# Performance work log

Hardware: AMD Instinct MI355X
Metric: run time of the kernel (lower is better)

The kernel has to match this reference:

```python
import jax, jax.numpy as jnp
import numpy as np

CUTOFF = 5.0
N_GAUSS = 25
LOG2 = 0.6931471805599453
N_INTER = 3


def ssp(x):
    # shifted softplus used by SchNet
    return jax.nn.softplus(x) - LOG2


def setup_inputs() -> dict:
    key = jax.random.key(0)
    ks = jax.random.split(key, 16)
    B, A, N, F, G, Z = 16, 128, 127, 128, N_GAUSS, 100
    s = 1.0 / np.sqrt(F)
    emb = jax.random.normal(ks[0], (Z, F), jnp.float32)
    emb = emb.at[0].set(0.0)  # padding_idx=0
    inp = {
        "positions": jax.random.normal(ks[1], (B, A, 3), jnp.float32) * 3.0,
        "cell": jnp.zeros((B, 3, 3), jnp.float32),
        "cell_offset": jnp.zeros((B, A, N, 3), jnp.float32),
        "neighbor_mask": jnp.ones((B, A, N), jnp.float32),
        "embeddings": emb,
        "filt_W1": jax.random.normal(ks[2], (N_INTER, G, F), jnp.float32) / np.sqrt(G),
        "filt_b1": jnp.zeros((N_INTER, F), jnp.float32),
        "filt_W2": jax.random.normal(ks[3], (N_INTER, F, F), jnp.float32) * s,
        "filt_b2": jnp.zeros((N_INTER, F), jnp.float32),
        "in2f_W": jax.random.normal(ks[4], (N_INTER, F, F), jnp.float32) * s,
        "f2out_W": jax.random.normal(ks[5], (N_INTER, F, F), jnp.float32) * s,
        "f2out_b": jnp.zeros((N_INTER, F), jnp.float32),
        "dense_W": jax.random.normal(ks[6], (N_INTER, F, F), jnp.float32) * s,
        "dense_b": jnp.zeros((N_INTER, F), jnp.float32),
        "atomic_numbers": jax.random.randint(ks[7], (B, A), 1, Z).astype(jnp.int32),
        "neighbors": jax.random.randint(ks[8], (B, A, N), 0, A).astype(jnp.int32),
    }
    return inp


def _schnet_forward(positions, cell, cell_offset, neighbor_mask, embeddings,
                    filt_W1, filt_b1, filt_W2, filt_b2,
                    in2f_W, f2out_W, f2out_b, dense_W, dense_b,
                    atomic_numbers, neighbors):
    B, A, _ = positions.shape
    bidx = jnp.arange(B)[:, None, None]

    # ---- AtomDistances: gather neighbor positions, pairwise distances ----
    pos_nbh = positions[bidx, neighbors]            # [B,A,N,3]
    dvec = pos_nbh - positions[:, :, None, :]
    dvec = dvec + jnp.einsum('banj,bjc->banc', cell_offset, cell)
    d2 = jnp.sum(dvec * dvec, axis=-1)              # [B,A,N]
    m = neighbor_mask > 0
    r_ij = jnp.where(m, jnp.sqrt(jnp.where(m, d2, 1.0)), 0.0)

    # ---- GaussianSmearing(0, cutoff, 25) ----
    centers = jnp.linspace(0.0, CUTOFF, N_GAUSS, dtype=r_ij.dtype)
    width = centers[1] - centers[0]
    coeff = -0.5 / (width * width)
    diff = r_ij[..., None] - centers                # [B,A,N,G]
    f_ij = jnp.exp(coeff * diff * diff)

    # ---- CosineCutoff ----
    C = 0.5 * (jnp.cos(r_ij * jnp.pi / CUTOFF) + 1.0)
    C = C * (r_ij < CUTOFF).astype(r_ij.dtype)      # [B,A,N]

    # ---- embedding ----
    x = embeddings[atomic_numbers]                  # [B,A,F]

    # ---- interaction blocks (cfconv + dense residual) ----
    for l in range(N_INTER):
        W = ssp(jnp.einsum('bang,gf->banf', f_ij, filt_W1[l]) + filt_b1[l])
        W = jnp.einsum('banf,fg->bang', W, filt_W2[l]) + filt_b2[l]
        W = W * C[..., None]                        # [B,A,N,F]
        y = x @ in2f_W[l]                           # [B,A,F], no bias
        y_nbh = y[bidx, neighbors]                  # [B,A,N,F]
        agg = jnp.sum(y_nbh * W * neighbor_mask[..., None], axis=2)  # [B,A,F]
        v = ssp(agg @ f2out_W[l] + f2out_b[l])
        v = v @ dense_W[l] + dense_b[l]
        x = x + v
    return x


def reference(positions, cell, cell_offset, neighbor_mask, embeddings,
              filt_W1, filt_b1, filt_W2, filt_b2,
              in2f_W, f2out_W, f2out_b, dense_W, dense_b,
              atomic_numbers, neighbors):
    return _schnet_forward(positions, cell, cell_offset, neighbor_mask, embeddings,
                           filt_W1, filt_b1, filt_W2, filt_b2,
                           in2f_W, f2out_W, f2out_b, dense_W, dense_b,
                           atomic_numbers, neighbors)
```

## Files before the change

kernel.cpp:

```cpp
#include <hip/hip_runtime.h>
#include <math.h>

#define BB 16
#define AA 128
#define NNB 127
#define FF 128
#define GG 25

typedef __attribute__((ext_vector_type(8))) short bf16x8;
typedef __attribute__((ext_vector_type(4))) float f32x4;
typedef unsigned short ushort_t;

__device__ __forceinline__ float ssp_f(float x) {
    return fmaxf(x, 0.f) + log1pf(__expf(-fabsf(x))) - 0.6931471805599453f;
}

__device__ __forceinline__ float ssp_fast(float x) {
    float e = __expf(-fabsf(x));
    float p = fmaf(e, 0.03215845f, -0.13606275f);
    p = fmaf(e, p, 0.28947478f);
    p = fmaf(e, p, -0.49190896f);
    p = fmaf(e, p, 0.99949556f);
    return fmaxf(x, 0.f) + e * p - 0.6931471805599453f;
}

__device__ __forceinline__ ushort_t f2bf(float f) {
    unsigned int u = __float_as_uint(f);
    unsigned int r = (u + 0x7fffu + ((u >> 16) & 1u)) >> 16;
    return (ushort_t)r;
}

__device__ __forceinline__ float bf2f(ushort_t h) {
    return __uint_as_float(((unsigned int)h) << 16);
}

__device__ __forceinline__ unsigned int pack2bf_rhu(float lo, float hi) {
    return __builtin_amdgcn_perm(__float_as_uint(hi) + 0x8000u,
                                 __float_as_uint(lo) + 0x8000u, 0x07060302u);
}

__global__ __launch_bounds__(256) void k_geom(const float* __restrict__ positions,
                                              const float* __restrict__ cell,
                                              const float* __restrict__ cell_offset,
                                              const float* __restrict__ nmask,
                                              const int* __restrict__ neighbors,
                                              float* __restrict__ r_g,
                                              float* __restrict__ cm_g) {
    int i = blockIdx.x * 256 + threadIdx.x;
    if (i >= BB * AA * 128) return;
    int row = i >> 7, n = i & 127;
    if (n < NNB) {
        int b = row >> 7;
        int nb = neighbors[row * NNB + n];
        float px = positions[row * 3 + 0], py = positions[row * 3 + 1], pz = positions[row * 3 + 2];
        int nrow = b * AA + nb;
        float qx = positions[nrow * 3 + 0], qy = positions[nrow * 3 + 1], qz = positions[nrow * 3 + 2];
        const float* co = cell_offset + (size_t)row * NNB * 3 + (size_t)n * 3;
        const float* cl = cell + b * 9;
        float c0 = co[0], c1 = co[1], c2 = co[2];
        float ox = c0 * cl[0] + c1 * cl[3] + c2 * cl[6];
        float oy = c0 * cl[1] + c1 * cl[4] + c2 * cl[7];
        float oz = c0 * cl[2] + c1 * cl[5] + c2 * cl[8];
        float dx = qx - px + ox, dy = qy - py + oy, dz = qz - pz + oz;
        float d2 = dx * dx + dy * dy + dz * dz;
        float mk = nmask[row * NNB + n];
        float r = (mk > 0.f) ? sqrtf(d2) : 0.f;
        float Cc = 0.5f * (__cosf(r * (3.14159265358979323846f / 5.0f)) + 1.f);
        Cc = (r < 5.0f) ? Cc : 0.f;
        r_g[i] = r;
        cm_g[i] = Cc * mk;
    } else {
        r_g[i] = 1e9f;
        cm_g[i] = 0.f;
    }
}

__global__ __launch_bounds__(256) void k_prep(const float* __restrict__ W1,
                                              const float* __restrict__ W2,
                                              const float* __restrict__ Win,
                                              const float* __restrict__ Wf,
                                              const float* __restrict__ Wd,
                                              ushort_t* __restrict__ w1t,
                                              ushort_t* __restrict__ w2f,
                                              ushort_t* __restrict__ whi,
                                              ushort_t* __restrict__ wlo) {
    int i = blockIdx.x * 256 + threadIdx.x;
    if (i < 3 * 128 * 32) {
        int l = i >> 12, rem = i & 4095, f = rem >> 5, g = rem & 31;
        float v = (g < GG) ? W1[l * GG * FF + g * FF + f] : 0.f;
        w1t[i] = f2bf(v);
    }
    if (i < 3 * 16384) {
        int l = i >> 14, e = i & 16383;
        int u = e >> 3, j = e & 7;
        int ks = u >> 9, rem = u & 511;
        int wcft = rem >> 6, lane = rem & 63;
        int f = (wcft >> 1) * 32 + (wcft & 1) * 16 + (lane & 15);
        int k = ks * 32 + (lane >> 4) * 8 + j;
        w2f[i] = f2bf(W2[l * 16384 + k * 128 + f]);
    }
    if (i < 9 * 16384) {
        int m = i / 49152;
        int rem = i - m * 49152;
        int l = rem >> 14;
        int rk = rem & 16383;
        int f = rk >> 7, k = rk & 127;
        const float* src = (m == 0) ? Win : ((m == 1) ? Wf : Wd);
        float v = src[l * 16384 + k * 128 + f];
        ushort_t h = f2bf(v);
        whi[i] = h;
        wlo[i] = f2bf(v - bf2f(h));
    }
}

__global__ __launch_bounds__(256) void k_init_x(const float* __restrict__ emb,
                                                const int* __restrict__ z,
                                                float* __restrict__ x) {
    int i = blockIdx.x * 256 + threadIdx.x;
    if (i < BB * AA * FF) {
        int row = i >> 7, f = i & 127;
        x[i] = emb[z[row] * FF + f];
    }
}

__global__ __launch_bounds__(512) void k_ffn(
    const float* __restrict__ agg, const float* __restrict__ x_in,
    float* __restrict__ x_out, float* __restrict__ y, float* __restrict__ out,
    const ushort_t* __restrict__ wfh, const ushort_t* __restrict__ wfl, const float* __restrict__ bfv_g,
    const ushort_t* __restrict__ wdh, const ushort_t* __restrict__ wdl, const float* __restrict__ bdv_g,
    const ushort_t* __restrict__ wih, const ushort_t* __restrict__ wil,
    int mode) {
    __shared__ ushort_t tsh[8][136];
    __shared__ ushort_t tsl[8][136];
    const int t = threadIdx.x;
    const int lane = t & 63, w = t >> 6;
    const int l15 = lane & 15, l4 = lane >> 4;
    const int r0 = blockIdx.x << 3;
    const int fcol = (w << 4) + l15;

    bf16x8 Ah[4], Al[4];

    auto loadA_global = [&](const float* __restrict__ M) {
#pragma unroll
        for (int ks = 0; ks < 4; ++ks) {
            float v[8];
            if (l15 < 8) {
                const float4* p = (const float4*)(M + ((size_t)(r0 + l15) << 7) + (ks << 5) + (l4 << 3));
                float4 a = p[0], b = p[1];
                v[0] = a.x; v[1] = a.y; v[2] = a.z; v[3] = a.w;
                v[4] = b.x; v[5] = b.y; v[6] = b.z; v[7] = b.w;
            } else {
#pragma unroll
                for (int j = 0; j < 8; ++j) v[j] = 0.f;
            }
#pragma unroll
            for (int j = 0; j < 8; ++j) {
                ushort_t h = f2bf(v[j]);
                Ah[ks][j] = (short)h;
                Al[ks][j] = (short)f2bf(v[j] - bf2f(h));
            }
        }
    };
    auto loadA_lds = [&]() {
#pragma unroll
        for (int ks = 0; ks < 4; ++ks) {
            if (l15 < 8) {
                const char* base = (const char*)&tsh[l15][0] + (ks << 6) + (l4 << 4);
                Ah[ks] = *(const bf16x8*)base;
                const char* basel = (const char*)&tsl[l15][0] + (ks << 6) + (l4 << 4);
                Al[ks] = *(const bf16x8*)basel;
            } else {
#pragma unroll
                for (int j = 0; j < 8; ++j) { Ah[ks][j] = 0; Al[ks][j] = 0; }
            }
        }
    };

    if (mode & 1) {
        loadA_global(agg);
        float bfv = bfv_g[fcol];
        f32x4 acc = {bfv, bfv, bfv, bfv};
#pragma unroll
        for (int ks = 0; ks < 4; ++ks) {
            const bf16x8 Bh = *(const bf16x8*)(wfh + ((size_t)fcol << 7) + (ks << 5) + (l4 << 3));
            const bf16x8 Bl = *(const bf16x8*)(wfl + ((size_t)fcol << 7) + (ks << 5) + (l4 << 3));
            acc = __builtin_amdgcn_mfma_f32_16x16x32_bf16(Al[ks], Bh, acc, 0, 0, 0);
            acc = __builtin_amdgcn_mfma_f32_16x16x32_bf16(Ah[ks], Bl, acc, 0, 0, 0);
            acc = __builtin_amdgcn_mfma_f32_16x16x32_bf16(Ah[ks], Bh, acc, 0, 0, 0);
        }
#pragma unroll
        for (int reg = 0; reg < 4; ++reg) {
            int r = (l4 << 2) + reg;
            if (r < 8) {
                float v = ssp_f(acc[reg]);
                ushort_t h = f2bf(v);
                tsh[r][fcol] = h;
                tsl[r][fcol] = f2bf(v - bf2f(h));
            }
        }
        __syncthreads();
        loadA_lds();
        float bdv = bdv_g[fcol];
        f32x4 acc2 = {bdv, bdv, bdv, bdv};
#pragma unroll
        for (int ks = 0; ks < 4; ++ks) {
            const bf16x8 Bh = *(const bf16x8*)(wdh + ((size_t)fcol << 7) + (ks << 5) + (l4 << 3));
            const bf16x8 Bl = *(const bf16x8*)(wdl + ((size_t)fcol << 7) + (ks << 5) + (l4 << 3));
            acc2 = __builtin_amdgcn_mfma_f32_16x16x32_bf16(Al[ks], Bh, acc2, 0, 0, 0);
            acc2 = __builtin_amdgcn_mfma_f32_16x16x32_bf16(Ah[ks], Bl, acc2, 0, 0, 0);
            acc2 = __builtin_amdgcn_mfma_f32_16x16x32_bf16(Ah[ks], Bh, acc2, 0, 0, 0);
        }
        __syncthreads();
#pragma unroll
        for (int reg = 0; reg < 4; ++reg) {
            int r = (l4 << 2) + reg;
            if (r < 8) {
                size_t gi = ((size_t)(r0 + r) << 7) + fcol;
                float xn = x_in[gi] + acc2[reg];
                x_out[gi] = xn;
                if (mode & 4) out[gi] = xn;
                if (mode & 2) {
                    ushort_t h = f2bf(xn);
                    tsh[r][fcol] = h;
                    tsl[r][fcol] = f2bf(xn - bf2f(h));
                }
            }
        }
        if (mode & 2) __syncthreads();
    }
    if (mode & 2) {
        if (mode & 1) loadA_lds(); else loadA_global(x_in);
        f32x4 acc3 = {0.f, 0.f, 0.f, 0.f};
#pragma unroll
        for (int ks = 0; ks < 4; ++ks) {
            const bf16x8 Bh = *(const bf16x8*)(wih + ((size_t)fcol << 7) + (ks << 5) + (l4 << 3));
            const bf16x8 Bl = *(const bf16x8*)(wil + ((size_t)fcol << 7) + (ks << 5) + (l4 << 3));
            acc3 = __builtin_amdgcn_mfma_f32_16x16x32_bf16(Al[ks], Bh, acc3, 0, 0, 0);
            acc3 = __builtin_amdgcn_mfma_f32_16x16x32_bf16(Ah[ks], Bl, acc3, 0, 0, 0);
            acc3 = __builtin_amdgcn_mfma_f32_16x16x32_bf16(Ah[ks], Bh, acc3, 0, 0, 0);
        }
#pragma unroll
        for (int reg = 0; reg < 4; ++reg) {
            int r = (l4 << 2) + reg;
            if (r < 8) y[((size_t)(r0 + r) << 7) + fcol] = acc3[reg];
        }
    }
}

#define SMEM_BYTES 34304

__global__ __launch_bounds__(512, 6) void k_cfconv(
    const float* __restrict__ r_g, const float* __restrict__ cm_g,
    const int* __restrict__ neighbors,
    const ushort_t* __restrict__ w1t, const float* __restrict__ b1,
    const ushort_t* __restrict__ w2f, const float* __restrict__ b2,
    const float* __restrict__ y, float* __restrict__ agg) {
    extern __shared__ char smem[];
    float* cm_s = (float*)(smem + 32768);
    int* nbr_s = (int*)(smem + 33280);
    float* r_s = (float*)(smem + 33792);
    float* red_s = (float*)smem;

    const int row = blockIdx.x;
    const int b = row >> 7;
    const int t = threadIdx.x;
    const int lane = t & 63, w = t >> 6;
    const int l15 = lane & 15, l4 = lane >> 4;
    const int wr = w >> 2, wc = w & 3;

    if (t < 128) {
        r_s[t] = r_g[((size_t)row << 7) + t];
        cm_s[t] = cm_g[((size_t)row << 7) + t];
        nbr_s[t] = (t < NNB) ? neighbors[row * NNB + t] : 0;
    }
    __syncthreads();

    {
        const int nrow = (w << 4) + l15;
        const float rv = r_s[nrow];
        const float width = 5.0f / (GG - 1);
        const float coeff = -0.5f / (width * width);
        float fv[8];
#pragma unroll
        for (int j = 0; j < 8; ++j) {
            int g = (l4 << 3) + j;
            float d = rv - g * width;
            fv[j] = (g < GG) ? __expf(coeff * d * d) : 0.f;
        }
        bf16x8 fb;
        unsigned int* fbu = (unsigned int*)&fb;
        fbu[0] = pack2bf_rhu(fv[0], fv[1]);
        fbu[1] = pack2bf_rhu(fv[2], fv[3]);
        fbu[2] = pack2bf_rhu(fv[4], fv[5]);
        fbu[3] = pack2bf_rhu(fv[6], fv[7]);
        const int base = nrow * 256;
        const int sw = (nrow & 7) << 4;
#pragma unroll
        for (int ft = 0; ft < 8; ++ft) {
            bf16x8 aw = *(const bf16x8*)(w1t + ((ft << 4) + l15) * 32 + (l4 << 3));
            const int f0 = (ft << 4) + (l4 << 2);
            f32x4 c0 = *(const f32x4*)(b1 + f0);
            f32x4 d = __builtin_amdgcn_mfma_f32_16x16x32_bf16(aw, fb, c0, 0, 0, 0);
            unsigned int lo32 = pack2bf_rhu(ssp_fast(d[0]), ssp_fast(d[1]));
            unsigned int hi32 = pack2bf_rhu(ssp_fast(d[2]), ssp_fast(d[3]));
            unsigned long long pk = (unsigned long long)lo32 | ((unsigned long long)hi32 << 32);
            *(unsigned long long*)(smem + base + ((f0 << 1) ^ sw)) = pk;
        }
    }

#define W2LD(ks, ft) (*(const bf16x8*)(w2f + (((((ks) << 3) + (wc << 1) + (ft)) << 6) + lane) * 8))
    bf16x8 wb0 = W2LD(0, 0), wb1 = W2LD(0, 1);
    __syncthreads();

    f32x4 acc[4][2];
#pragma unroll
    for (int mi = 0; mi < 4; ++mi)
#pragma unroll
        for (int ft = 0; ft < 2; ++ft) {
            float b2v = b2[(wc << 5) + (ft << 4) + l15];
            f32x4 c0 = {b2v, b2v, b2v, b2v};
            acc[mi][ft] = c0;
        }
#pragma unroll
    for (int ks = 0; ks < 4; ++ks) {
        bf16x8 wn0, wn1;
        if (ks < 3) { wn0 = W2LD(ks + 1, 0); wn1 = W2LD(ks + 1, 1); }
        bf16x8 ha[4];
#pragma unroll
        for (int mi = 0; mi < 4; ++mi) {
            int n = (wr << 6) + (mi << 4) + l15;
            ha[mi] = *(const bf16x8*)(smem + n * 256 + ((((ks << 2) + l4) << 4) ^ ((n & 7) << 4)));
        }
#pragma unroll
        for (int mi = 0; mi < 4; ++mi) {
            acc[mi][0] = __builtin_amdgcn_mfma_f32_16x16x32_bf16(ha[mi], wb0, acc[mi][0], 0, 0, 0);
            acc[mi][1] = __builtin_amdgcn_mfma_f32_16x16x32_bf16(ha[mi], wb1, acc[mi][1], 0, 0, 0);
        }
        if (ks < 3) { wb0 = wn0; wb1 = wn1; }
    }
#undef W2LD
    __syncthreads();

    float part0 = 0.f, part1 = 0.f;
    const float* ybase = y + ((size_t)(b * AA) << 7) + (wc << 5) + l15;
#pragma unroll
    for (int mi = 0; mi < 4; ++mi) {
        float yv0[4], yv1[4], cmv[4];
#pragma unroll
        for (int r = 0; r < 4; ++r) {
            int n = (wr << 6) + (mi << 4) + (l4 << 2) + r;
            int nb = nbr_s[n];
            cmv[r] = cm_s[n];
            const float* yr = ybase + ((size_t)nb << 7);
            yv0[r] = yr[0];
            yv1[r] = yr[16];
        }
#pragma unroll
        for (int r = 0; r < 4; ++r) {
            part0 = fmaf(yv0[r], acc[mi][0][r] * cmv[r], part0);
            part1 = fmaf(yv1[r], acc[mi][1][r] * cmv[r], part1);
        }
    }
    {
        int xg = l4 << 3;
        red_s[(w << 7) + (l4 << 5) + (l15 ^ xg)] = part0;
        red_s[(w << 7) + (l4 << 5) + ((16 + l15) ^ xg)] = part1;
    }
    __syncthreads();
    if (t < FF) {
        int wcf = t >> 5, fl = t & 31;
        float s = 0.f;
#pragma unroll
        for (int wr2 = 0; wr2 < 2; ++wr2)
#pragma unroll
            for (int g = 0; g < 4; ++g)
                s += red_s[(((wr2 << 2) + wcf) << 7) + (g << 5) + (fl ^ (g << 3))];
        agg[(size_t)row * FF + t] = s;
    }
}

extern "C" void kernel_launch(void* const* d_in, const int* in_sizes, int n_in,
                              void* d_out, int out_size, void* d_ws, size_t ws_size,
                              hipStream_t stream) {
    const float* positions   = (const float*)d_in[0];
    const float* cell        = (const float*)d_in[1];
    const float* cell_offset = (const float*)d_in[2];
    const float* nmask       = (const float*)d_in[3];
    const float* emb         = (const float*)d_in[4];
    const float* filt_W1     = (const float*)d_in[5];
    const float* filt_b1     = (const float*)d_in[6];
    const float* filt_W2     = (const float*)d_in[7];
    const float* filt_b2     = (const float*)d_in[8];
    const float* in2f_W      = (const float*)d_in[9];
    const float* f2out_W     = (const float*)d_in[10];
    const float* f2out_b     = (const float*)d_in[11];
    const float* dense_W     = (const float*)d_in[12];
    const float* dense_b     = (const float*)d_in[13];
    const int* atomic_numbers = (const int*)d_in[14];
    const int* neighbors      = (const int*)d_in[15];
    float* out = (float*)d_out;

    float* x    = (float*)d_ws;
    float* yb   = x + BB * AA * FF;
    float* agg  = yb + BB * AA * FF;
    float* r_g  = agg + BB * AA * FF;
    float* cm_g = r_g + BB * AA * 128;
    ushort_t* w1t = (ushort_t*)(cm_g + BB * AA * 128);
    ushort_t* w2f = w1t + 3 * 128 * 32;
    ushort_t* whi = w2f + 3 * 16384;
    ushort_t* wlo = whi + 9 * 16384;

    k_geom<<<(BB * AA * 128 + 255) / 256, 256, 0, stream>>>(positions, cell, cell_offset,
                                                            nmask, neighbors, r_g, cm_g);
    k_prep<<<576, 256, 0, stream>>>(filt_W1, filt_W2, in2f_W, f2out_W, dense_W,
                                    w1t, w2f, whi, wlo);
    k_init_x<<<(BB * AA * FF + 255) / 256, 256, 0, stream>>>(emb, atomic_numbers, x);

    k_ffn<<<256, 512, 0, stream>>>(x, x, x, yb, out,
                                   whi + 3 * 16384, wlo + 3 * 16384, f2out_b,
                                   whi + 6 * 16384, wlo + 6 * 16384, dense_b,
                                   whi + 0 * 16384, wlo + 0 * 16384,
                                   2);
    for (int l = 0; l < 3; ++l) {
        k_cfconv<<<BB * AA, 512, SMEM_BYTES, stream>>>(
            r_g, cm_g, neighbors,
            w1t + (size_t)l * 128 * 32, filt_b1 + (size_t)l * FF,
            w2f + (size_t)l * 16384, filt_b2 + (size_t)l * FF,
            yb, agg);
        int nextl = (l < 2) ? (l + 1) : 0;
        int mode = 1 | ((l < 2) ? 2 : 0) | ((l == 2) ? 4 : 0);
        k_ffn<<<256, 512, 0, stream>>>(agg, x, x, yb, out,
                                       whi + (3 + l) * 16384, wlo + (3 + l) * 16384, f2out_b + (size_t)l * FF,
                                       whi + (6 + l) * 16384, wlo + (6 + l) * 16384, dense_b + (size_t)l * FF,
                                       whi + nextl * 16384, wlo + nextl * 16384,
                                       mode);
    }
}
```

Measured before the change: 126.7 us.

## Fuse setup kernels and interleave y columns for paired neighbor gathers

Merges the geometry, weight-prep and embedding-init kernels into one setup launch. The k_ffn y output is stored with a column permutation so each k_cfconv lane fetches its two feature columns with one float2 load, and the neighbor indices and cutoff values come in as one int4 and one float4 LDS read. It also drops the r staging in shared memory and one barrier by reading r directly from global. This trims launch overhead and gather instruction count, but the cm/nbr shared loads now rely on the later barrier for ordering.

```diff
diff --git a/kernel.cpp b/kernel.cpp
--- a/kernel.cpp
+++ b/kernel.cpp
@@ -39,52 +39,51 @@
                                  __float_as_uint(lo) + 0x8000u, 0x07060302u);
 }
 
-__global__ __launch_bounds__(256) void k_geom(const float* __restrict__ positions,
-                                              const float* __restrict__ cell,
-                                              const float* __restrict__ cell_offset,
-                                              const float* __restrict__ nmask,
-                                              const int* __restrict__ neighbors,
-                                              float* __restrict__ r_g,
-                                              float* __restrict__ cm_g) {
+__device__ __forceinline__ int yperm(int f) {
+    return (f & ~31) + ((f & 15) << 1) + ((f >> 4) & 1);
+}
+
+__global__ __launch_bounds__(256) void k_setup(
+    const float* __restrict__ positions, const float* __restrict__ cell,
+    const float* __restrict__ cell_offset, const float* __restrict__ nmask,
+    const int* __restrict__ neighbors,
+    const float* __restrict__ W1, const float* __restrict__ W2,
+    const float* __restrict__ Win, const float* __restrict__ Wf, const float* __restrict__ Wd,
+    const float* __restrict__ emb, const int* __restrict__ z,
+    float* __restrict__ r_g, float* __restrict__ cm_g,
+    ushort_t* __restrict__ w1t, ushort_t* __restrict__ w2f,
+    ushort_t* __restrict__ whi, ushort_t* __restrict__ wlo,
+    float* __restrict__ x) {
     int i = blockIdx.x * 256 + threadIdx.x;
-    if (i >= BB * AA * 128) return;
-    int row = i >> 7, n = i & 127;
-    if (n < NNB) {
-        int b = row >> 7;
-        int nb = neighbors[row * NNB + n];
-        float px = positions[row * 3 + 0], py = positions[row * 3 + 1], pz = positions[row * 3 + 2];
-        int nrow = b * AA + nb;
-        float qx = positions[nrow * 3 + 0], qy = positions[nrow * 3 + 1], qz = positions[nrow * 3 + 2];
-        const float* co = cell_offset + (size_t)row * NNB * 3 + (size_t)n * 3;
-        const float* cl = cell + b * 9;
-        float c0 = co[0], c1 = co[1], c2 = co[2];
-        float ox = c0 * cl[0] + c1 * cl[3] + c2 * cl[6];
-        float oy = c0 * cl[1] + c1 * cl[4] + c2 * cl[7];
-        float oz = c0 * cl[2] + c1 * cl[5] + c2 * cl[8];
-        float dx = qx - px + ox, dy = qy - py + oy, dz = qz - pz + oz;
-        float d2 = dx * dx + dy * dy + dz * dz;
-        float mk = nmask[row * NNB + n];
-        float r = (mk > 0.f) ? sqrtf(d2) : 0.f;
-        float Cc = 0.5f * (__cosf(r * (3.14159265358979323846f / 5.0f)) + 1.f);
-        Cc = (r < 5.0f) ? Cc : 0.f;
-        r_g[i] = r;
-        cm_g[i] = Cc * mk;
-    } else {
-        r_g[i] = 1e9f;
-        cm_g[i] = 0.f;
-    }
-}
-
-__global__ __launch_bounds__(256) void k_prep(const float* __restrict__ W1,
-                                              const float* __restrict__ W2,
-                                              const float* __restrict__ Win,
-                                              const float* __restrict__ Wf,
-                                              const float* __restrict__ Wd,
-                                              ushort_t* __restrict__ w1t,
-                                              ushort_t* __restrict__ w2f,
-                                              ushort_t* __restrict__ whi,
-                                              ushort_t* __restrict__ wlo) {
-    int i = blockIdx.x * 256 + threadIdx.x;
+    if (i < BB * AA * 128) {
+        int row = i >> 7, n = i & 127;
+        if (n < NNB) {
+            int b = row >> 7;
+            int nb = neighbors[row * NNB + n];
+            float px = positions[row * 3 + 0], py = positions[row * 3 + 1], pz = positions[row * 3 + 2];
+            int nrow = b * AA + nb;
+            float qx = positions[nrow * 3 + 0], qy = positions[nrow * 3 + 1], qz = positions[nrow * 3 + 2];
+            const float* co = cell_offset + (size_t)row * NNB * 3 + (size_t)n * 3;
+            const float* cl = cell + b * 9;
+            float c0 = co[0], c1 = co[1], c2 = co[2];
+            float ox = c0 * cl[0] + c1 * cl[3] + c2 * cl[6];
+            float oy = c0 * cl[1] + c1 * cl[4] + c2 * cl[7];
+            float oz = c0 * cl[2] + c1 * cl[5] + c2 * cl[8];
+            float dx = qx - px + ox, dy = qy - py + oy, dz = qz - pz + oz;
+            float d2 = dx * dx + dy * dy + dz * dz;
+            float mk = nmask[row * NNB + n];
+            float r = (mk > 0.f) ? sqrtf(d2) : 0.f;
+            float Cc = 0.5f * (__cosf(r * (3.14159265358979323846f / 5.0f)) + 1.f);
+            Cc = (r < 5.0f) ? Cc : 0.f;
+            r_g[i] = r;
+            cm_g[i] = Cc * mk;
+        } else {
+            r_g[i] = 1e9f;
+            cm_g[i] = 0.f;
+        }
+        int f = i & 127;
+        x[i] = emb[z[i >> 7] * FF + f];
+    }
     if (i < 3 * 128 * 32) {
         int l = i >> 12, rem = i & 4095, f = rem >> 5, g = rem & 31;
         float v = (g < GG) ? W1[l * GG * FF + g * FF + f] : 0.f;
@@ -110,16 +109,6 @@
         ushort_t h = f2bf(v);
         whi[i] = h;
         wlo[i] = f2bf(v - bf2f(h));
-    }
-}
-
-__global__ __launch_bounds__(256) void k_init_x(const float* __restrict__ emb,
-                                                const int* __restrict__ z,
-                                                float* __restrict__ x) {
-    int i = blockIdx.x * 256 + threadIdx.x;
-    if (i < BB * AA * FF) {
-        int row = i >> 7, f = i & 127;
-        x[i] = emb[z[row] * FF + f];
     }
 }
 
@@ -239,15 +228,16 @@
             acc3 = __builtin_amdgcn_mfma_f32_16x16x32_bf16(Ah[ks], Bl, acc3, 0, 0, 0);
             acc3 = __builtin_amdgcn_mfma_f32_16x16x32_bf16(Ah[ks], Bh, acc3, 0, 0, 0);
         }
+        const int pf = yperm(fcol);
 #pragma unroll
         for (int reg = 0; reg < 4; ++reg) {
             int r = (l4 << 2) + reg;
-            if (r < 8) y[((size_t)(r0 + r) << 7) + fcol] = acc3[reg];
-        }
-    }
-}
-
-#define SMEM_BYTES 34304
+            if (r < 8) y[((size_t)(r0 + r) << 7) + pf] = acc3[reg];
+        }
+    }
+}
+
+#define SMEM_BYTES 33792
 
 __global__ __launch_bounds__(512, 6) void k_cfconv(
     const float* __restrict__ r_g, const float* __restrict__ cm_g,
@@ -258,7 +248,6 @@
     extern __shared__ char smem[];
     float* cm_s = (float*)(smem + 32768);
     int* nbr_s = (int*)(smem + 33280);
-    float* r_s = (float*)(smem + 33792);
     float* red_s = (float*)smem;
 
     const int row = blockIdx.x;
@@ -269,15 +258,13 @@
     const int wr = w >> 2, wc = w & 3;
 
     if (t < 128) {
-        r_s[t] = r_g[((size_t)row << 7) + t];
         cm_s[t] = cm_g[((size_t)row << 7) + t];
         nbr_s[t] = (t < NNB) ? neighbors[row * NNB + t] : 0;
     }
-    __syncthreads();
 
     {
         const int nrow = (w << 4) + l15;
-        const float rv = r_s[nrow];
+        const float rv = r_g[((size_t)row << 7) + nrow];
         const float width = 5.0f / (GG - 1);
         const float coeff = -0.5f / (width * width);
         float fv[8];
@@ -342,24 +329,24 @@
     __syncthreads();
 
     float part0 = 0.f, part1 = 0.f;
-    const float* ybase = y + ((size_t)(b * AA) << 7) + (wc << 5) + l15;
+    const float* ybase = y + ((size_t)(b * AA) << 7) + (wc << 5) + (l15 << 1);
 #pragma unroll
     for (int mi = 0; mi < 4; ++mi) {
-        float yv0[4], yv1[4], cmv[4];
-#pragma unroll
-        for (int r = 0; r < 4; ++r) {
-            int n = (wr << 6) + (mi << 4) + (l4 << 2) + r;
-            int nb = nbr_s[n];
-            cmv[r] = cm_s[n];
-            const float* yr = ybase + ((size_t)nb << 7);
-            yv0[r] = yr[0];
-            yv1[r] = yr[16];
-        }
-#pragma unroll
-        for (int r = 0; r < 4; ++r) {
-            part0 = fmaf(yv0[r], acc[mi][0][r] * cmv[r], part0);
-            part1 = fmaf(yv1[r], acc[mi][1][r] * cmv[r], part1);
-        }
+        int n0 = (wr << 6) + (mi << 4) + (l4 << 2);
+        float4 cmv = *(const float4*)(cm_s + n0);
+        int4 nb4 = *(const int4*)(nbr_s + n0);
+        float2 y0 = *(const float2*)(ybase + ((size_t)nb4.x << 7));
+        float2 y1 = *(const float2*)(ybase + ((size_t)nb4.y << 7));
+        float2 y2 = *(const float2*)(ybase + ((size_t)nb4.z << 7));
+        float2 y3 = *(const float2*)(ybase + ((size_t)nb4.w << 7));
+        part0 = fmaf(y0.x, acc[mi][0][0] * cmv.x, part0);
+        part1 = fmaf(y0.y, acc[mi][1][0] * cmv.x, part1);
+        part0 = fmaf(y1.x, acc[mi][0][1] * cmv.y, part0);
+        part1 = fmaf(y1.y, acc[mi][1][1] * cmv.y, part1);
+        part0 = fmaf(y2.x, acc[mi][0][2] * cmv.z, part0);
+        part1 = fmaf(y2.y, acc[mi][1][2] * cmv.z, part1);
+        part0 = fmaf(y3.x, acc[mi][0][3] * cmv.w, part0);
+        part1 = fmaf(y3.y, acc[mi][1][3] * cmv.w, part1);
     }
     {
         int xg = l4 << 3;
@@ -410,11 +397,10 @@
     ushort_t* whi = w2f + 3 * 16384;
     ushort_t* wlo = whi + 9 * 16384;
 
-    k_geom<<<(BB * AA * 128 + 255) / 256, 256, 0, stream>>>(positions, cell, cell_offset,
-                                                            nmask, neighbors, r_g, cm_g);
-    k_prep<<<576, 256, 0, stream>>>(filt_W1, filt_W2, in2f_W, f2out_W, dense_W,
-                                    w1t, w2f, whi, wlo);
-    k_init_x<<<(BB * AA * FF + 255) / 256, 256, 0, stream>>>(emb, atomic_numbers, x);
+    k_setup<<<1024, 256, 0, stream>>>(positions, cell, cell_offset, nmask, neighbors,
+                                      filt_W1, filt_W2, in2f_W, f2out_W, dense_W,
+                                      emb, atomic_numbers,
+                                      r_g, cm_g, w1t, w2f, whi, wlo, x);
 
     k_ffn<<<256, 512, 0, stream>>>(x, x, x, yb, out,
                                    whi + 3 * 16384, wlo + 3 * 16384, f2out_b,
```

Result: slower. 129.8 us (+2.4%).
